# Kernel tuning notes

Hardware: AMD Instinct MI355X
Metric: run time of the kernel (lower is better)

Reference implementation:

```python
import jax, jax.numpy as jnp
import numpy as np

B, T, P, D, S, R = 4, 128, 256, 512, 64, 8  # batch, window, patches, d_model, n_state, dt_rank


def setup_inputs() -> dict:
    key = jax.random.key(0)
    ks = jax.random.split(key, 8)
    sc = 0.02  # weight init scale
    return {
        "X": jax.random.normal(ks[0], (B, T, P, D), jnp.float32),
        "H0": jnp.zeros((B, P, S), jnp.float32),
        "a_hat": jax.random.normal(ks[1], (S,), jnp.float32),
        "U_w": jax.random.normal(ks[2], (S, D), jnp.float32) * sc,
        "sB_w": jax.random.normal(ks[3], (S, D), jnp.float32) * sc,
        "sB_b": jnp.zeros((S,), jnp.float32),
        "sC_w": jax.random.normal(ks[4], (S, D), jnp.float32) * sc,
        "sC_b": jnp.zeros((S,), jnp.float32),
        "sD1_w": jax.random.normal(ks[5], (R, D), jnp.float32) * sc,
        "sD1_b": jnp.zeros((R,), jnp.float32),
        "sD2_w": jax.random.normal(ks[6], (1, R), jnp.float32) * sc,
        "sD2_b": jnp.zeros((1,), jnp.float32),
        "ro_w": jax.random.normal(ks[7], (D, S), jnp.float32) * sc,
    }


def reference(X, H0, a_hat, U_w, sB_w, sB_b, sC_w, sC_b, sD1_w, sD1_b, sD2_w, sD2_b, ro_w):
    eps = 1e-12
    logA = -jnp.exp(a_hat)                                    # [S]
    # selective (input-dependent) parameters
    u = jnp.einsum('btpd,sd->btps', X, U_w)                   # [B,T,P,S]
    B_t = jnp.einsum('btpd,sd->btps', X, sB_w) + sB_b
    C_t = jnp.einsum('btpd,sd->btps', X, sC_w) + sC_b
    dt_feat = jax.nn.silu(jnp.einsum('btpd,rd->btpr', X, sD1_w) + sD1_b)
    dt = jax.nn.softplus(jnp.einsum('btpr,or->btpo', dt_feat, sD2_w) + sD2_b)  # [B,T,P,1]
    A = jnp.exp(dt * logA)                                    # [B,T,P,S] via broadcast
    b = (1.0 - A) * (B_t * u)
    # prefix-product scan: h_t = A_t*h_{t-1} + b_t  ->  h_t = P_t*(H0 + cumsum(b/P))
    Pc = jnp.cumprod(jnp.maximum(A, eps), axis=1)             # [B,T,P,S]
    invP = 1.0 / jnp.maximum(Pc, eps)
    c = jnp.cumsum(b * invP, axis=1)
    H_seq = Pc * (H0[:, None] + c)                            # [B,T,P,S]
    Y_seq = jnp.einsum('btps,ds->btpd', C_t * H_seq, ro_w)    # [B,T,P,D]
    Y_seq = Y_seq.reshape(X.shape[0], -1, X.shape[-1])        # [B, T*P, D]
    H_T = H_seq[:, -1]                                        # [B,P,S]
    return (H_seq, Y_seq, H_T)
```

## Files before the change

kernel.cpp:

```cpp
#include <hip/hip_runtime.h>
#include <hip/hip_bf16.h>
#include <math.h>

namespace {
constexpr int B_N = 4, T_N = 128, P_N = 256, D_N = 512, S_N = 64;
constexpr int NTH = 512;
constexpr int KC  = 32;
constexpr int NCH = D_N / KC;

constexpr int XS_OFF  = 0;
constexpr int WS_OFF  = 8192;
constexpr int BU_OFF  = 0;
constexpr int CH_OFF  = 16384;
constexpr int ROS_OFF = 0;
constexpr int DT_OFF  = 32768;
constexpr int LA_OFF  = 33280;
constexpr int LDS_BYTES = 33536;
}

typedef short bf16x8 __attribute__((ext_vector_type(8)));
typedef float f32x4  __attribute__((ext_vector_type(4)));

__device__ __forceinline__ unsigned short f2b(float f) {
    unsigned int x = __float_as_uint(f);
    return (unsigned short)((x + 0x7FFFu + ((x >> 16) & 1u)) >> 16);
}
__device__ __forceinline__ float b2f(unsigned short h) {
    return __uint_as_float(((unsigned int)h) << 16);
}
__device__ __forceinline__ unsigned int pk2(float lo, float hi) {
    union { __hip_bfloat162 h; unsigned int u; } cv;
    cv.h = __float22bfloat162_rn(float2{lo, hi});
    return cv.u;
}
__device__ __forceinline__ int swz32(int row, int col) {
    return row * 32 + (col ^ (((row >> 1) & 3) << 3));
}
__device__ __forceinline__ int swz64(int row, int col) {
    return row * 64 + (col ^ ((row & 7) << 3));
}
__device__ __forceinline__ void cvtstore8(unsigned short* dst, float4 a, float4 b) {
    uint4 r;
    r.x = pk2(a.x, a.y); r.y = pk2(a.z, a.w);
    r.z = pk2(b.x, b.y); r.w = pk2(b.z, b.w);
    *(uint4*)dst = r;
}

__global__ __launch_bounds__(NTH, 4) void mamba_mfma(
    const float* __restrict__ X, const float* __restrict__ H0,
    const float* __restrict__ a_hat,
    const float* __restrict__ U_w, const float* __restrict__ sB_w, const float* __restrict__ sB_b,
    const float* __restrict__ sC_w, const float* __restrict__ sC_b,
    const float* __restrict__ sD1_w, const float* __restrict__ sD1_b,
    const float* __restrict__ sD2_w, const float* __restrict__ sD2_b,
    const float* __restrict__ ro_w,
    float* __restrict__ Hseq, float* __restrict__ Y, float* __restrict__ HT)
{
    __shared__ __align__(16) char smem[LDS_BYTES];
    unsigned short* XS  = (unsigned short*)(smem + XS_OFF);
    unsigned short* WS  = (unsigned short*)(smem + WS_OFF);
    unsigned short* BU  = (unsigned short*)(smem + BU_OFF);
    unsigned short* ROS = (unsigned short*)(smem + ROS_OFF);
    unsigned short* CHB = (unsigned short*)(smem + CH_OFF);
    float*          DTB = (float*)(smem + DT_OFF);
    float*          LA  = (float*)(smem + LA_OFF);

    const int tid  = threadIdx.x;
    const int lane = tid & 63;
    const int wid  = tid >> 6;
    const int wm   = wid >> 2;
    const int wn   = wid & 3;
    const int l15  = lane & 15;
    const int lg   = lane >> 4;
    const int b    = blockIdx.x >> 8;
    const int p    = blockIdx.x & 255;

    if (tid < S_N) LA[tid] = -expf(a_hat[tid]);
    if (tid < 128) ((unsigned int*)(WS + 200 * 32))[tid] = 0;

    f32x4 acc[4][3];
    f32x4 accdt;
    #pragma unroll
    for (int q = 0; q < 4; ++q) accdt[q] = 0.0f;
    #pragma unroll
    for (int mf = 0; mf < 4; ++mf)
        #pragma unroll
        for (int nf = 0; nf < 3; ++nf)
            #pragma unroll
            for (int q = 0; q < 4; ++q) acc[mf][nf][q] = 0.0f;

    const int xr = tid >> 2, xq = tid & 3;
    const float* xsrc = X + (((size_t)b * T_N + xr) * P_N + p) * D_N + xq * 8;
    unsigned short* xdst = &XS[swz32(xr, xq * 8)];

    const int wr0 = tid >> 2, wq = tid & 3;
    const int wr1 = 128 + wr0;
    const bool hasW1 = (tid < 288);
    const float* wsrc0;
    {
        int g = wr0 >> 4, w = wr0 & 15, tr = g % 3, sb = g / 3;
        const float* base = (tr == 0) ? U_w : (tr == 1) ? sB_w : sC_w;
        wsrc0 = base + (size_t)(sb * 16 + w) * D_N + wq * 8;
    }
    const float* wsrc1;
    if (wr1 < 192) {
        int g = wr1 >> 4, w = wr1 & 15, tr = g % 3, sb = g / 3;
        const float* base = (tr == 0) ? U_w : (tr == 1) ? sB_w : sC_w;
        wsrc1 = base + (size_t)(sb * 16 + w) * D_N + wq * 8;
    } else if (wr1 < 200) {
        wsrc1 = sD1_w + (size_t)(wr1 - 192) * D_N + wq * 8;
    } else {
        wsrc1 = wsrc0;
    }
    unsigned short* wdst0 = &WS[swz32(wr0, wq * 8)];
    unsigned short* wdst1 = &WS[swz32(wr1 < 208 ? wr1 : 0, wq * 8)];

    float4 xA = *(const float4*)(xsrc),  xB = *(const float4*)(xsrc + 4);
    float4 wA0 = *(const float4*)(wsrc0), wB0 = *(const float4*)(wsrc0 + 4);
    float4 wA1 = *(const float4*)(wsrc1), wB1 = *(const float4*)(wsrc1 + 4);

    const int kb = lg * 8;
    for (int kc = 0; kc < NCH; ++kc) {
        cvtstore8(xdst, xA, xB);
        cvtstore8(wdst0, wA0, wB0);
        if (hasW1) cvtstore8(wdst1, wA1, wB1);
        __syncthreads();
        if (kc + 1 < NCH) {
            const float* nx = xsrc + (kc + 1) * KC;
            xA = *(const float4*)(nx); xB = *(const float4*)(nx + 4);
            const float* n0 = wsrc0 + (kc + 1) * KC;
            wA0 = *(const float4*)(n0); wB0 = *(const float4*)(n0 + 4);
            const float* n1 = wsrc1 + (kc + 1) * KC;
            wA1 = *(const float4*)(n1); wB1 = *(const float4*)(n1 + 4);
        }
        bf16x8 a[4];
        #pragma unroll
        for (int mf = 0; mf < 4; ++mf)
            a[mf] = *(const bf16x8*)&XS[swz32(wm * 64 + mf * 16 + l15, kb)];
        #pragma unroll
        for (int nf = 0; nf < 3; ++nf) {
            bf16x8 bb = *(const bf16x8*)&WS[swz32(wn * 48 + nf * 16 + l15, kb)];
            #pragma unroll
            for (int mf = 0; mf < 4; ++mf)
                acc[mf][nf] = __builtin_amdgcn_mfma_f32_16x16x32_bf16(a[mf], bb, acc[mf][nf], 0, 0, 0);
        }
        {
            bf16x8 adt = *(const bf16x8*)&XS[swz32(wid * 16 + l15, kb)];
            bf16x8 bd  = *(const bf16x8*)&WS[swz32(192 + l15, kb)];
            accdt = __builtin_amdgcn_mfma_f32_16x16x32_bf16(adt, bd, accdt, 0, 0, 0);
        }
        __syncthreads();
    }

    {
        const int s = wn * 16 + l15;
        const float biasB = sB_b[s], biasC = sC_b[s];
        #pragma unroll
        for (int mf = 0; mf < 4; ++mf) {
            #pragma unroll
            for (int q = 0; q < 4; ++q) {
                const int t = wm * 64 + mf * 16 + lg * 4 + q;
                const float u  = acc[mf][0][q];
                const float Bv = acc[mf][1][q] + biasB;
                const float Cv = acc[mf][2][q] + biasC;
                BU[t * 64 + s]   = f2b(Bv * u);
                CHB[swz64(t, s)] = f2b(Cv);
            }
        }
    }
    {
        const float w2 = (l15 < 8) ? sD2_w[l15] : 0.0f;
        const float b1 = (l15 < 8) ? sD1_b[l15] : 0.0f;
        const float b2 = sD2_b[0];
        #pragma unroll
        for (int q = 0; q < 4; ++q) {
            float z = accdt[q] + b1;
            float w = (z / (1.0f + expf(-z))) * w2;
            w = (l15 < 8) ? w : 0.0f;
            w += __shfl_xor(w, 1);
            w += __shfl_xor(w, 2);
            w += __shfl_xor(w, 4);
            if (l15 == 0) {
                float zz = w + b2;
                DTB[wid * 16 + lg * 4 + q] = (zz > 20.0f) ? zz : log1pf(expf(zz));
            }
        }
    }
    __syncthreads();

    const int rrow = tid >> 2, rq = tid & 3;
    const float* rosrc = ro_w + (size_t)rrow * S_N + rq * 16;
    float4 r0a = *(const float4*)(rosrc);
    float4 r0b = *(const float4*)(rosrc + 4);
    float4 r0c = *(const float4*)(rosrc + 8);
    float4 r0d = *(const float4*)(rosrc + 12);

    if (tid < 64) {
        const int s = tid;
        const float la = LA[s];
        const float h0 = H0[((size_t)b * P_N + p) * S_N + s];
        float Pcv = 1.0f, cv = 0.0f, Hv = 0.0f;
        float* hout = Hseq + ((size_t)b * T_N * P_N + p) * S_N + s;
        for (int t = 0; t < T_N; ++t) {
            const float Av = expf(DTB[t] * la);
            const float bv = (1.0f - Av) * b2f(BU[t * 64 + s]);
            Pcv *= fmaxf(Av, 1e-12f);
            cv += bv * (1.0f / fmaxf(Pcv, 1e-12f));
            Hv = Pcv * (h0 + cv);
            hout[(size_t)t * P_N * S_N] = Hv;
            const int e = swz64(t, s);
            CHB[e] = f2b(b2f(CHB[e]) * Hv);
        }
        HT[((size_t)b * P_N + p) * S_N + s] = Hv;
    }
    __syncthreads();

    bf16x8 af0[4], af1[4];
    #pragma unroll
    for (int mf = 0; mf < 4; ++mf) {
        af0[mf] = *(const bf16x8*)&CHB[swz64(wm * 64 + mf * 16 + l15, lg * 8)];
        af1[mf] = *(const bf16x8*)&CHB[swz64(wm * 64 + mf * 16 + l15, 32 + lg * 8)];
    }
    cvtstore8(&ROS[swz64(rrow, rq * 16)],     r0a, r0b);
    cvtstore8(&ROS[swz64(rrow, rq * 16 + 8)], r0c, r0d);
    __syncthreads();

    for (int pp = 0; pp < 4; ++pp) {
        if (pp < 3) {
            const float* ns = ro_w + (size_t)((pp + 1) * 128 + rrow) * S_N + rq * 16;
            r0a = *(const float4*)(ns);
            r0b = *(const float4*)(ns + 4);
            r0c = *(const float4*)(ns + 8);
            r0d = *(const float4*)(ns + 12);
        }
        f32x4 yacc[4][2];
        #pragma unroll
        for (int mf = 0; mf < 4; ++mf)
            #pragma unroll
            for (int nf = 0; nf < 2; ++nf)
                #pragma unroll
                for (int q = 0; q < 4; ++q) yacc[mf][nf][q] = 0.0f;
        #pragma unroll
        for (int nf = 0; nf < 2; ++nf) {
            bf16x8 bb0 = *(const bf16x8*)&ROS[swz64(wn * 32 + nf * 16 + l15, lg * 8)];
            bf16x8 bb1 = *(const bf16x8*)&ROS[swz64(wn * 32 + nf * 16 + l15, 32 + lg * 8)];
            #pragma unroll
            for (int mf = 0; mf < 4; ++mf) {
                yacc[mf][nf] = __builtin_amdgcn_mfma_f32_16x16x32_bf16(af0[mf], bb0, yacc[mf][nf], 0, 0, 0);
                yacc[mf][nf] = __builtin_amdgcn_mfma_f32_16x16x32_bf16(af1[mf], bb1, yacc[mf][nf], 0, 0, 0);
            }
        }
        #pragma unroll
        for (int mf = 0; mf < 4; ++mf) {
            const int t0 = wm * 64 + mf * 16 + lg * 4;
            float* ybase = Y + (((size_t)b * T_N + t0) * P_N + p) * D_N + pp * 128 + wn * 32 + l15;
            #pragma unroll
            for (int nf = 0; nf < 2; ++nf) {
                #pragma unroll
                for (int q = 0; q < 4; ++q)
                    ybase[(size_t)q * P_N * D_N + nf * 16] = yacc[mf][nf][q];
            }
        }
        __syncthreads();
        if (pp < 3) {
            cvtstore8(&ROS[swz64(rrow, rq * 16)],     r0a, r0b);
            cvtstore8(&ROS[swz64(rrow, rq * 16 + 8)], r0c, r0d);
            __syncthreads();
        }
    }
}

extern "C" void kernel_launch(void* const* d_in, const int* in_sizes, int n_in,
                              void* d_out, int out_size, void* d_ws, size_t ws_size,
                              hipStream_t stream) {
    const float* X     = (const float*)d_in[0];
    const float* H0    = (const float*)d_in[1];
    const float* a_hat = (const float*)d_in[2];
    const float* U_w   = (const float*)d_in[3];
    const float* sB_w  = (const float*)d_in[4];
    const float* sB_b  = (const float*)d_in[5];
    const float* sC_w  = (const float*)d_in[6];
    const float* sC_b  = (const float*)d_in[7];
    const float* sD1_w = (const float*)d_in[8];
    const float* sD1_b = (const float*)d_in[9];
    const float* sD2_w = (const float*)d_in[10];
    const float* sD2_b = (const float*)d_in[11];
    const float* ro_w  = (const float*)d_in[12];

    float* out   = (float*)d_out;
    float* HseqP = out;
    float* YP    = out + (size_t)B_N * T_N * P_N * S_N;
    float* HTP   = YP  + (size_t)B_N * T_N * P_N * D_N;

    hipLaunchKernelGGL(mamba_mfma, dim3(B_N * P_N), dim3(NTH), 0, stream,
                       X, H0, a_hat, U_w, sB_w, sB_b, sC_w, sC_b,
                       sD1_w, sD1_b, sD2_w, sD2_b, ro_w, HseqP, YP, HTP);
}
```

Before: 159.6 us.

## Double-buffer LDS tiles in projection GEMM loop with one barrier per chunk

```diff
diff --git a/kernel.cpp b/kernel.cpp
--- a/kernel.cpp
+++ b/kernel.cpp
@@ -8,14 +8,15 @@
 constexpr int KC  = 32;
 constexpr int NCH = D_N / KC;
 
-constexpr int XS_OFF  = 0;
-constexpr int WS_OFF  = 8192;
+constexpr int XS0_OFF = 0;
+constexpr int WS0_OFF = 8192;
+constexpr int XS1_OFF = 21504;
+constexpr int WS1_OFF = 29696;
 constexpr int BU_OFF  = 0;
 constexpr int CH_OFF  = 16384;
 constexpr int ROS_OFF = 0;
-constexpr int DT_OFF  = 32768;
-constexpr int LA_OFF  = 33280;
-constexpr int LDS_BYTES = 33536;
+constexpr int DT_OFF  = 43008;
+constexpr int LDS_BYTES = 43520;
 }
 
 typedef short bf16x8 __attribute__((ext_vector_type(8)));
@@ -57,13 +58,14 @@
     float* __restrict__ Hseq, float* __restrict__ Y, float* __restrict__ HT)
 {
     __shared__ __align__(16) char smem[LDS_BYTES];
-    unsigned short* XS  = (unsigned short*)(smem + XS_OFF);
-    unsigned short* WS  = (unsigned short*)(smem + WS_OFF);
+    unsigned short* XS0 = (unsigned short*)(smem + XS0_OFF);
+    unsigned short* WS0 = (unsigned short*)(smem + WS0_OFF);
+    unsigned short* XS1 = (unsigned short*)(smem + XS1_OFF);
+    unsigned short* WS1 = (unsigned short*)(smem + WS1_OFF);
     unsigned short* BU  = (unsigned short*)(smem + BU_OFF);
     unsigned short* ROS = (unsigned short*)(smem + ROS_OFF);
     unsigned short* CHB = (unsigned short*)(smem + CH_OFF);
     float*          DTB = (float*)(smem + DT_OFF);
-    float*          LA  = (float*)(smem + LA_OFF);
 
     const int tid  = threadIdx.x;
     const int lane = tid & 63;
@@ -75,8 +77,13 @@
     const int b    = blockIdx.x >> 8;
     const int p    = blockIdx.x & 255;
 
-    if (tid < S_N) LA[tid] = -expf(a_hat[tid]);
-    if (tid < 128) ((unsigned int*)(WS + 200 * 32))[tid] = 0;
+    const float la  = (tid < 64) ? -expf(a_hat[tid]) : 0.0f;
+    const float h0v = (tid < 64) ? H0[((size_t)b * P_N + p) * S_N + tid] : 0.0f;
+
+    if (tid < 128) {
+        ((unsigned int*)(WS0 + 200 * 32))[tid] = 0;
+        ((unsigned int*)(WS1 + 200 * 32))[tid] = 0;
+    }
 
     f32x4 acc[4][3];
     f32x4 accdt;
@@ -91,7 +98,7 @@
 
     const int xr = tid >> 2, xq = tid & 3;
     const float* xsrc = X + (((size_t)b * T_N + xr) * P_N + p) * D_N + xq * 8;
-    unsigned short* xdst = &XS[swz32(xr, xq * 8)];
+    const int xoff = swz32(xr, xq * 8);
 
     const int wr0 = tid >> 2, wq = tid & 3;
     const int wr1 = 128 + wr0;
@@ -112,43 +119,63 @@
     } else {
         wsrc1 = wsrc0;
     }
-    unsigned short* wdst0 = &WS[swz32(wr0, wq * 8)];
-    unsigned short* wdst1 = &WS[swz32(wr1 < 208 ? wr1 : 0, wq * 8)];
-
-    float4 xA = *(const float4*)(xsrc),  xB = *(const float4*)(xsrc + 4);
+    const int woff0 = swz32(wr0, wq * 8);
+    const int woff1 = swz32(wr1 < 208 ? wr1 : 0, wq * 8);
+
+    float4 xA = *(const float4*)(xsrc),   xB = *(const float4*)(xsrc + 4);
     float4 wA0 = *(const float4*)(wsrc0), wB0 = *(const float4*)(wsrc0 + 4);
     float4 wA1 = *(const float4*)(wsrc1), wB1 = *(const float4*)(wsrc1 + 4);
+    cvtstore8(&XS0[xoff],  xA, xB);
+    cvtstore8(&WS0[woff0], wA0, wB0);
+    if (hasW1) cvtstore8(&WS0[woff1], wA1, wB1);
+    {
+        const float* nx = xsrc + KC;
+        xA = *(const float4*)(nx); xB = *(const float4*)(nx + 4);
+        const float* n0 = wsrc0 + KC;
+        wA0 = *(const float4*)(n0); wB0 = *(const float4*)(n0 + 4);
+        const float* n1 = wsrc1 + KC;
+        wA1 = *(const float4*)(n1); wB1 = *(const float4*)(n1 + 4);
+    }
+    __syncthreads();
 
     const int kb = lg * 8;
+    #pragma unroll 2
     for (int kc = 0; kc < NCH; ++kc) {
-        cvtstore8(xdst, xA, xB);
-        cvtstore8(wdst0, wA0, wB0);
-        if (hasW1) cvtstore8(wdst1, wA1, wB1);
-        __syncthreads();
+        unsigned short* XSc = (kc & 1) ? XS1 : XS0;
+        unsigned short* WSc = (kc & 1) ? WS1 : WS0;
+        unsigned short* XSn = (kc & 1) ? XS0 : XS1;
+        unsigned short* WSn = (kc & 1) ? WS0 : WS1;
         if (kc + 1 < NCH) {
-            const float* nx = xsrc + (kc + 1) * KC;
+            cvtstore8(&XSn[xoff],  xA, xB);
+            cvtstore8(&WSn[woff0], wA0, wB0);
+            if (hasW1) cvtstore8(&WSn[woff1], wA1, wB1);
+        }
+        if (kc + 2 < NCH) {
+            const float* nx = xsrc + (kc + 2) * KC;
             xA = *(const float4*)(nx); xB = *(const float4*)(nx + 4);
-            const float* n0 = wsrc0 + (kc + 1) * KC;
+            const float* n0 = wsrc0 + (kc + 2) * KC;
             wA0 = *(const float4*)(n0); wB0 = *(const float4*)(n0 + 4);
-            const float* n1 = wsrc1 + (kc + 1) * KC;
+            const float* n1 = wsrc1 + (kc + 2) * KC;
             wA1 = *(const float4*)(n1); wB1 = *(const float4*)(n1 + 4);
         }
+        __builtin_amdgcn_s_setprio(1);
         bf16x8 a[4];
         #pragma unroll
         for (int mf = 0; mf < 4; ++mf)
-            a[mf] = *(const bf16x8*)&XS[swz32(wm * 64 + mf * 16 + l15, kb)];
+            a[mf] = *(const bf16x8*)&XSc[swz32(wm * 64 + mf * 16 + l15, kb)];
         #pragma unroll
         for (int nf = 0; nf < 3; ++nf) {
-            bf16x8 bb = *(const bf16x8*)&WS[swz32(wn * 48 + nf * 16 + l15, kb)];
+            bf16x8 bb = *(const bf16x8*)&WSc[swz32(wn * 48 + nf * 16 + l15, kb)];
             #pragma unroll
             for (int mf = 0; mf < 4; ++mf)
                 acc[mf][nf] = __builtin_amdgcn_mfma_f32_16x16x32_bf16(a[mf], bb, acc[mf][nf], 0, 0, 0);
         }
         {
-            bf16x8 adt = *(const bf16x8*)&XS[swz32(wid * 16 + l15, kb)];
-            bf16x8 bd  = *(const bf16x8*)&WS[swz32(192 + l15, kb)];
+            bf16x8 adt = *(const bf16x8*)&XSc[swz32(wid * 16 + l15, kb)];
+            bf16x8 bd  = *(const bf16x8*)&WSc[swz32(192 + l15, kb)];
             accdt = __builtin_amdgcn_mfma_f32_16x16x32_bf16(adt, bd, accdt, 0, 0, 0);
         }
+        __builtin_amdgcn_s_setprio(0);
         __syncthreads();
     }
 
@@ -197,8 +224,6 @@
 
     if (tid < 64) {
         const int s = tid;
-        const float la = LA[s];
-        const float h0 = H0[((size_t)b * P_N + p) * S_N + s];
         float Pcv = 1.0f, cv = 0.0f, Hv = 0.0f;
         float* hout = Hseq + ((size_t)b * T_N * P_N + p) * S_N + s;
         for (int t = 0; t < T_N; ++t) {
@@ -206,7 +231,7 @@
             const float bv = (1.0f - Av) * b2f(BU[t * 64 + s]);
             Pcv *= fmaxf(Av, 1e-12f);
             cv += bv * (1.0f / fmaxf(Pcv, 1e-12f));
-            Hv = Pcv * (h0 + cv);
+            Hv = Pcv * (h0v + cv);
             hout[(size_t)t * P_N * S_N] = Hv;
             const int e = swz64(t, s);
             CHB[e] = f2b(b2f(CHB[e]) * Hv);
```

Measured after the change: 156.5 us. 2.0% less time.
